# Kernel optimization log

Hardware: AMD Instinct MI355X
Metric: run time of the kernel (lower is better)

Reference implementation:

```python
import jax, jax.numpy as jnp
import numpy as np


def _qrnn_forward(X, W, b):
    seq_len, batch, d = X.shape
    H = W.shape[0] // 3
    Y = jnp.einsum('sbd,hd->sbh', X, W) + b  # [S,B,3H]
    Z, F, O = jnp.split(Y, 3, axis=2)
    Z = jnp.tanh(Z)
    F = jax.nn.sigmoid(F)

    # ForgetMult with hidden_init=None: h_0 = f_0*z_0; h_t = f_t*z_t + (1-f_t)*h_{t-1}
    # Equivalent to scan from h_{-1} = 0.
    def step(h_prev, fz):
        f_t, z_t = fz
        h = f_t * z_t + (1.0 - f_t) * h_prev
        return h, h

    h0 = jnp.zeros((batch, H), dtype=X.dtype)
    _, C = jax.lax.scan(step, h0, (F, Z))  # [S,B,H]
    Hout = jax.nn.sigmoid(O) * C
    return Hout, C[-1:, :, :]


def setup_inputs() -> dict:
    key = jax.random.key(0)
    k1, k2, k3 = jax.random.split(key, 3)
    S, B, D, Hdim = 1024, 16, 1024, 1024
    X = jax.random.normal(k1, (S, B, D), dtype=jnp.float32)
    W = jax.random.normal(k2, (3 * Hdim, D), dtype=jnp.float32) * (1.0 / np.sqrt(D))
    b = jax.random.normal(k3, (3 * Hdim,), dtype=jnp.float32) * 0.01
    return {"X": X, "W": W, "b": b}


def reference(X, W, b):
    return _qrnn_forward(X, W, b)
```

## Files before the change

### kernel.cpp

```cpp
#include <hip/hip_runtime.h>
#include <hip/hip_bf16.h>
#include <stdint.h>

typedef __bf16 bf16x8 __attribute__((ext_vector_type(8)));
typedef float f32x4 __attribute__((ext_vector_type(4)));

constexpr int S = 1024, Bsz = 16, Hd = 1024;
constexpr int M = S * Bsz;
constexpr int N = 3 * Hd;
constexpr int K = 1024;
constexpr int BM = 128, BN = 128, BK = 32;

__device__ __forceinline__ float fast_sigmoid(float x) { return 1.0f / (1.0f + __expf(-x)); }
__device__ __forceinline__ float fast_tanh(float x) { return 2.0f / (1.0f + __expf(-2.0f * x)) - 1.0f; }

__device__ __forceinline__ void gld_lds16(const __bf16* g, __bf16* l) {
  __builtin_amdgcn_global_load_lds(
      (const __attribute__((address_space(1))) void*)g,
      (__attribute__((address_space(3))) void*)l,
      16, 0, 0);
}

__global__ void convert_f32_bf16(const float* __restrict__ src, __bf16* __restrict__ dst, int n8) {
  int i = blockIdx.x * blockDim.x + threadIdx.x;
  if (i >= n8) return;
  const float4* s4 = (const float4*)src;
  float4 a = s4[2 * i], b = s4[2 * i + 1];
  bf16x8 v;
  v[0] = (__bf16)a.x; v[1] = (__bf16)a.y; v[2] = (__bf16)a.z; v[3] = (__bf16)a.w;
  v[4] = (__bf16)b.x; v[5] = (__bf16)b.y; v[6] = (__bf16)b.z; v[7] = (__bf16)b.w;
  *((bf16x8*)dst + i) = v;
}

template <typename T>
__global__ __launch_bounds__(256) void gemm_act(const __bf16* __restrict__ A,
                                                const __bf16* __restrict__ Bw,
                                                const float* __restrict__ bias,
                                                T* __restrict__ Y) {
  __shared__ __align__(16) __bf16 As[BM * BK];
  __shared__ __align__(16) __bf16 Bs[BN * BK];
  const int t = threadIdx.x;
  const int lane = t & 63;
  const int wave = t >> 6;
  const int wm = wave >> 1, wn = wave & 1;
  const int tn = blockIdx.x % (N / BN);
  const int tm = blockIdx.x / (N / BN);
  const int m0 = tm * BM, n0 = tn * BN;
  const int lrow = lane & 15;
  const int quad = lane >> 4;

  const int srow = t >> 2;
  const int scw = t & 3;
  const __bf16* gA0 = A + (size_t)(m0 + srow) * K + scw * 8;
  const __bf16* gA1 = gA0 + (size_t)64 * K;
  const __bf16* gB0 = Bw + (size_t)(n0 + srow) * K + scw * 8;
  const __bf16* gB1 = gB0 + (size_t)64 * K;
  __bf16* lA0 = As + wave * 512;
  __bf16* lA1 = As + 2048 + wave * 512;
  __bf16* lB0 = Bs + wave * 512;
  __bf16* lB1 = Bs + 2048 + wave * 512;

  f32x4 acc[4][4] = {};

  for (int k0 = 0; k0 < K; k0 += BK) {
    __syncthreads();
    gld_lds16(gA0, lA0);
    gld_lds16(gA1, lA1);
    gld_lds16(gB0, lB0);
    gld_lds16(gB1, lB1);
    gA0 += BK; gA1 += BK; gB0 += BK; gB1 += BK;
    __syncthreads();

    bf16x8 af[4], bfr[4];
#pragma unroll
    for (int mi = 0; mi < 4; ++mi)
      af[mi] = *(const bf16x8*)(&As[(wm * 64 + mi * 16 + lrow) * BK + quad * 8]);
#pragma unroll
    for (int ni = 0; ni < 4; ++ni)
      bfr[ni] = *(const bf16x8*)(&Bs[(wn * 64 + ni * 16 + lrow) * BK + quad * 8]);
#pragma unroll
    for (int mi = 0; mi < 4; ++mi)
#pragma unroll
      for (int ni = 0; ni < 4; ++ni)
        acc[mi][ni] = __builtin_amdgcn_mfma_f32_16x16x32_bf16(af[mi], bfr[ni], acc[mi][ni], 0, 0, 0);
  }

#pragma unroll
  for (int ni = 0; ni < 4; ++ni) {
    int col = n0 + wn * 64 + ni * 16 + lrow;
    float bv = bias[col];
    bool is_tanh = (col < Hd);
#pragma unroll
    for (int mi = 0; mi < 4; ++mi) {
#pragma unroll
      for (int r = 0; r < 4; ++r) {
        int m = m0 + wm * 64 + mi * 16 + quad * 4 + r;
        float y = acc[mi][ni][r] + bv;
        float v = is_tanh ? fast_tanh(y) : fast_sigmoid(y);
        Y[(size_t)m * N + col] = (T)v;
      }
    }
  }
}

template <typename T>
__global__ __launch_bounds__(64) void qrnn_scan(const T* __restrict__ Y,
                                                float* __restrict__ hout,
                                                float* __restrict__ clast) {
  int tid = blockIdx.x * blockDim.x + threadIdx.x;
  int b = tid >> 10, h = tid & 1023;
  const size_t sstep = (size_t)Bsz * N;
  size_t zoff = (size_t)b * N + h;
  size_t ooff = (size_t)b * Hd + h;
  float hp = 0.0f;
  constexpr int DEPTH = 16;
  for (int s0 = 0; s0 < S; s0 += DEPTH) {
    float z[DEPTH], f[DEPTH], o[DEPTH];
#pragma unroll
    for (int j = 0; j < DEPTH; ++j) {
      size_t base = zoff + (size_t)(s0 + j) * sstep;
      z[j] = (float)Y[base];
      f[j] = (float)Y[base + Hd];
      o[j] = (float)Y[base + 2 * Hd];
    }
#pragma unroll
    for (int j = 0; j < DEPTH; ++j) {
      hp = f[j] * z[j] + (1.0f - f[j]) * hp;
      hout[ooff + (size_t)(s0 + j) * (Bsz * Hd)] = o[j] * hp;
    }
  }
  clast[tid] = hp;
}

extern "C" void kernel_launch(void* const* d_in, const int* in_sizes, int n_in,
                              void* d_out, int out_size, void* d_ws, size_t ws_size,
                              hipStream_t stream) {
  const float* X = (const float*)d_in[0];
  const float* W = (const float*)d_in[1];
  const float* bias = (const float*)d_in[2];
  float* out = (float*)d_out;

  char* ws = (char*)d_ws;
  __bf16* Xb = (__bf16*)ws;
  __bf16* Wb = (__bf16*)(ws + 33554432);
  void* Yv = (void*)(ws + 33554432 + 6291456);

  const size_t need_f32 = 39845888ull + (size_t)M * N * 4ull;
  bool yf32 = (ws_size >= need_f32);

  convert_f32_bf16<<<8192, 256, 0, stream>>>(X, Xb, 2097152);
  convert_f32_bf16<<<1536, 256, 0, stream>>>(W, Wb, 393216);

  dim3 ggrid((M / BM) * (N / BN));
  if (yf32) {
    gemm_act<float><<<ggrid, 256, 0, stream>>>(Xb, Wb, bias, (float*)Yv);
    qrnn_scan<float><<<256, 64, 0, stream>>>((const float*)Yv, out, out + 16777216);
  } else {
    gemm_act<__bf16><<<ggrid, 256, 0, stream>>>(Xb, Wb, bias, (__bf16*)Yv);
    qrnn_scan<__bf16><<<256, 64, 0, stream>>>((const __bf16*)Yv, out, out + 16777216);
  }
}
```

Baseline: 374.2 us.

## Parallelize QRNN scan across sequence chunks and swizzle GEMM LDS layout

Replaces the single-pass sequential scan, which used only 16K threads, with a three-pass chunked scan. Pass 1 computes per-chunk affine (A,B) coefficients over 32 chunks, pass 2 scans the chunk carries, and pass 3 recomputes the outputs with the carried-in state. This raises parallelism 32x for the memory-bound recurrence, at the cost of reading Z and F twice and adding scratch buffers and extra launches. It also XOR-swizzles the GEMM's LDS layout to reduce bank conflicts on fragment reads.

```diff
diff --git a/kernel.cpp b/kernel.cpp
--- a/kernel.cpp
+++ b/kernel.cpp
@@ -10,6 +10,8 @@
 constexpr int N = 3 * Hd;
 constexpr int K = 1024;
 constexpr int BM = 128, BN = 128, BK = 32;
+constexpr int NCH = 32, CS = S / NCH;
+constexpr int BH = Bsz * Hd;
 
 __device__ __forceinline__ float fast_sigmoid(float x) { return 1.0f / (1.0f + __expf(-x)); }
 __device__ __forceinline__ float fast_tanh(float x) { return 2.0f / (1.0f + __expf(-2.0f * x)) - 1.0f; }
@@ -50,15 +52,19 @@
   const int quad = lane >> 4;
 
   const int srow = t >> 2;
-  const int scw = t & 3;
-  const __bf16* gA0 = A + (size_t)(m0 + srow) * K + scw * 8;
-  const __bf16* gA1 = gA0 + (size_t)64 * K;
-  const __bf16* gB0 = Bw + (size_t)(n0 + srow) * K + scw * 8;
-  const __bf16* gB1 = gB0 + (size_t)64 * K;
+  const int cw_store = t & 3;
+  const int sswz = (srow ^ (srow >> 2)) & 3;
+  const int cw_log = cw_store ^ sswz;
+  const __bf16* gA0 = A + (size_t)(m0 + srow) * K + cw_log * 8;
+  const __bf16* gA1 = A + (size_t)(m0 + srow + 64) * K + cw_log * 8;
+  const __bf16* gB0 = Bw + (size_t)(n0 + srow) * K + cw_log * 8;
+  const __bf16* gB1 = Bw + (size_t)(n0 + srow + 64) * K + cw_log * 8;
   __bf16* lA0 = As + wave * 512;
   __bf16* lA1 = As + 2048 + wave * 512;
   __bf16* lB0 = Bs + wave * 512;
   __bf16* lB1 = Bs + 2048 + wave * 512;
+
+  const int rswz = (lrow ^ (lrow >> 2)) & 3;
 
   f32x4 acc[4][4] = {};
 
@@ -74,10 +80,10 @@
     bf16x8 af[4], bfr[4];
 #pragma unroll
     for (int mi = 0; mi < 4; ++mi)
-      af[mi] = *(const bf16x8*)(&As[(wm * 64 + mi * 16 + lrow) * BK + quad * 8]);
+      af[mi] = *(const bf16x8*)(&As[(wm * 64 + mi * 16 + lrow) * BK + ((quad ^ rswz) * 8)]);
 #pragma unroll
     for (int ni = 0; ni < 4; ++ni)
-      bfr[ni] = *(const bf16x8*)(&Bs[(wn * 64 + ni * 16 + lrow) * BK + quad * 8]);
+      bfr[ni] = *(const bf16x8*)(&Bs[(wn * 64 + ni * 16 + lrow) * BK + ((quad ^ rswz) * 8)]);
 #pragma unroll
     for (int mi = 0; mi < 4; ++mi)
 #pragma unroll
@@ -104,32 +110,76 @@
 }
 
 template <typename T>
-__global__ __launch_bounds__(64) void qrnn_scan(const T* __restrict__ Y,
-                                                float* __restrict__ hout,
-                                                float* __restrict__ clast) {
-  int tid = blockIdx.x * blockDim.x + threadIdx.x;
-  int b = tid >> 10, h = tid & 1023;
+__global__ __launch_bounds__(256) void scan_pass1(const T* __restrict__ Y,
+                                                  float* __restrict__ Ac,
+                                                  float* __restrict__ Bc) {
+  int tid = blockIdx.x * 256 + threadIdx.x;
+  int c = tid >> 14;
+  int bh = tid & (BH - 1);
+  int b = bh >> 10, h = bh & (Hd - 1);
   const size_t sstep = (size_t)Bsz * N;
-  size_t zoff = (size_t)b * N + h;
-  size_t ooff = (size_t)b * Hd + h;
-  float hp = 0.0f;
-  constexpr int DEPTH = 16;
-  for (int s0 = 0; s0 < S; s0 += DEPTH) {
-    float z[DEPTH], f[DEPTH], o[DEPTH];
-#pragma unroll
-    for (int j = 0; j < DEPTH; ++j) {
-      size_t base = zoff + (size_t)(s0 + j) * sstep;
+  size_t base0 = (size_t)b * N + h + (size_t)(c * CS) * sstep;
+  float A = 1.0f, B = 0.0f;
+  for (int j0 = 0; j0 < CS; j0 += 8) {
+    float z[8], f[8];
+#pragma unroll
+    for (int j = 0; j < 8; ++j) {
+      size_t base = base0 + (size_t)(j0 + j) * sstep;
+      z[j] = (float)Y[base];
+      f[j] = (float)Y[base + Hd];
+    }
+#pragma unroll
+    for (int j = 0; j < 8; ++j) {
+      float a = 1.0f - f[j];
+      B = fmaf(a, B, f[j] * z[j]);
+      A *= a;
+    }
+  }
+  Ac[tid] = A;
+  Bc[tid] = B;
+}
+
+__global__ __launch_bounds__(256) void scan_pass2(const float* __restrict__ Ac,
+                                                  const float* __restrict__ Bc,
+                                                  float* __restrict__ hin,
+                                                  float* __restrict__ clast) {
+  int bh = blockIdx.x * 256 + threadIdx.x;
+  float h = 0.0f;
+#pragma unroll 4
+  for (int c = 0; c < NCH; ++c) {
+    hin[c * BH + bh] = h;
+    h = fmaf(Ac[c * BH + bh], h, Bc[c * BH + bh]);
+  }
+  clast[bh] = h;
+}
+
+template <typename T>
+__global__ __launch_bounds__(256) void scan_pass3(const T* __restrict__ Y,
+                                                  const float* __restrict__ hin,
+                                                  float* __restrict__ hout) {
+  int tid = blockIdx.x * 256 + threadIdx.x;
+  int c = tid >> 14;
+  int bh = tid & (BH - 1);
+  int b = bh >> 10, h = bh & (Hd - 1);
+  const size_t sstep = (size_t)Bsz * N;
+  size_t base0 = (size_t)b * N + h + (size_t)(c * CS) * sstep;
+  size_t obase = (size_t)b * Hd + h + (size_t)(c * CS) * BH;
+  float hp = hin[tid];
+  for (int j0 = 0; j0 < CS; j0 += 8) {
+    float z[8], f[8], o[8];
+#pragma unroll
+    for (int j = 0; j < 8; ++j) {
+      size_t base = base0 + (size_t)(j0 + j) * sstep;
       z[j] = (float)Y[base];
       f[j] = (float)Y[base + Hd];
       o[j] = (float)Y[base + 2 * Hd];
     }
 #pragma unroll
-    for (int j = 0; j < DEPTH; ++j) {
-      hp = f[j] * z[j] + (1.0f - f[j]) * hp;
-      hout[ooff + (size_t)(s0 + j) * (Bsz * Hd)] = o[j] * hp;
-    }
-  }
-  clast[tid] = hp;
+    for (int j = 0; j < 8; ++j) {
+      hp = fmaf(f[j], z[j] - hp, hp);
+      hout[obase + (size_t)(j0 + j) * BH] = o[j] * hp;
+    }
+  }
 }
 
 extern "C" void kernel_launch(void* const* d_in, const int* in_sizes, int n_in,
@@ -143,20 +193,34 @@
   char* ws = (char*)d_ws;
   __bf16* Xb = (__bf16*)ws;
   __bf16* Wb = (__bf16*)(ws + 33554432);
-  void* Yv = (void*)(ws + 33554432 + 6291456);
-
-  const size_t need_f32 = 39845888ull + (size_t)M * N * 4ull;
-  bool yf32 = (ws_size >= need_f32);
+  char* Yp = ws + 39845888;
+
+  const size_t y_f32 = (size_t)M * N * 4ull;
+  const size_t y_bf16 = (size_t)M * N * 2ull;
+  const size_t scratch = 3ull * NCH * BH * 4ull;
+  bool yf32 = (ws_size >= 39845888ull + y_f32 + scratch);
+
+  size_t ybytes = yf32 ? y_f32 : y_bf16;
+  float* Ac = (float*)(Yp + ybytes);
+  float* Bc = Ac + NCH * BH;
+  float* hin = Bc + NCH * BH;
 
   convert_f32_bf16<<<8192, 256, 0, stream>>>(X, Xb, 2097152);
   convert_f32_bf16<<<1536, 256, 0, stream>>>(W, Wb, 393216);
 
   dim3 ggrid((M / BM) * (N / BN));
+  dim3 sgrid(NCH * BH / 256);
   if (yf32) {
-    gemm_act<float><<<ggrid, 256, 0, stream>>>(Xb, Wb, bias, (float*)Yv);
-    qrnn_scan<float><<<256, 64, 0, stream>>>((const float*)Yv, out, out + 16777216);
+    float* Yv = (float*)Yp;
+    gemm_act<float><<<ggrid, 256, 0, stream>>>(Xb, Wb, bias, Yv);
+    scan_pass1<float><<<sgrid, 256, 0, stream>>>(Yv, Ac, Bc);
+    scan_pass2<<<BH / 256, 256, 0, stream>>>(Ac, Bc, hin, out + 16777216);
+    scan_pass3<float><<<sgrid, 256, 0, stream>>>(Yv, hin, out);
   } else {
-    gemm_act<__bf16><<<ggrid, 256, 0, stream>>>(Xb, Wb, bias, (__bf16*)Yv);
-    qrnn_scan<__bf16><<<256, 64, 0, stream>>>((const __bf16*)Yv, out, out + 16777216);
-  }
-}
+    __bf16* Yv = (__bf16*)Yp;
+    gemm_act<__bf16><<<ggrid, 256, 0, stream>>>(Xb, Wb, bias, Yv);
+    scan_pass1<__bf16><<<sgrid, 256, 0, stream>>>(Yv, Ac, Bc);
+    scan_pass2<<<BH / 256, 256, 0, stream>>>(Ac, Bc, hin, out + 16777216);
+    scan_pass3<__bf16><<<sgrid, 256, 0, stream>>>(Yv, hin, out);
+  }
+}
```

Result: faster. 335.4 us (-10.4%).
